# Kernel optimization log

Hardware: AMD Instinct MI355X
Metric: run time of the kernel (lower is better)

The kernel has to match this reference:

```python
import jax, jax.numpy as jnp
import numpy as np

HIDDEN = 4544
N_HEADS = 71
HEAD_DIM = 64
ROPE_BASE = 10000.0


def _rope_cos_sin(pos, dtype):
    # Falcon rotary embedding for a single decode position `pos`.
    inv_freq = 1.0 / (ROPE_BASE ** (jnp.arange(0, HEAD_DIM, 2, dtype=jnp.float32) / HEAD_DIM))
    freqs = pos * inv_freq                      # [HEAD_DIM/2]
    emb = jnp.concatenate([freqs, freqs])       # [HEAD_DIM]
    return jnp.cos(emb).astype(dtype), jnp.sin(emb).astype(dtype)


def _rotate_half(x):
    x1, x2 = jnp.split(x, 2, axis=-1)
    return jnp.concatenate([-x2, x1], axis=-1)


def setup_inputs() -> dict:
    key = jax.random.key(0)
    ks = jax.random.split(key, 6)
    B = 32
    return {
        "hidden_states": jax.random.normal(ks[0], (1, 1, B, HIDDEN), jnp.float32) * 0.02,
        "attention_mask": jnp.zeros((B, 1, 1, 2048), jnp.float32),
        "w_qkv": jax.random.normal(ks[1], (HIDDEN, (N_HEADS + 2) * HEAD_DIM), jnp.float32) * 0.02,
        "w_dense": jax.random.normal(ks[2], (HIDDEN, HIDDEN), jnp.float32) * 0.02,
        "k_cache": jax.random.normal(ks[3], (B, 1, 2048, HEAD_DIM), jnp.float32),
        "v_cache": jax.random.normal(ks[4], (B, 1, 2048, HEAD_DIM), jnp.float32),
        "layer_past_len": 2047,
    }


def reference(hidden_states, attention_mask, w_qkv, w_dense, k_cache, v_cache, layer_past_len):
    B = hidden_states.shape[2]
    kv_len = layer_past_len + 1
    scalar = 1.0 / np.sqrt(HEAD_DIM)

    x = hidden_states.reshape(B, HIDDEN)                    # decode: [1,1,B,H] -> [B,H]
    qkv = x @ w_qkv                                          # [B, (nh+2)*hd]
    q = qkv[:, : N_HEADS * HEAD_DIM].reshape(B, N_HEADS, HEAD_DIM)
    k = qkv[:, N_HEADS * HEAD_DIM : (N_HEADS + 1) * HEAD_DIM]  # [B, hd] (single MQA KV head)
    v = qkv[:, (N_HEADS + 1) * HEAD_DIM :]                     # [B, hd]

    cos, sin = _rope_cos_sin(jnp.float32(layer_past_len), qkv.dtype)
    q = q * cos + _rotate_half(q) * sin                      # [B, nh, hd]
    k = k * cos + _rotate_half(k) * sin                      # [B, hd]

    # KV-cache scatter update at position layer_past_len
    k_cache = k_cache.at[:, 0, layer_past_len, :].set(k)
    v_cache = v_cache.at[:, 0, layer_past_len, :].set(v)

    keys = k_cache[:, 0, :kv_len, :]                         # [B, L, hd]
    vals = v_cache[:, 0, :kv_len, :]                         # [B, L, hd]

    scores = jnp.einsum("bnh,blh->bnl", q, keys) * scalar    # [B, nh, L]
    scores = scores + attention_mask[:, 0, :, :kv_len]       # mask [B,1,L] broadcast over heads
    probs = jax.nn.softmax(scores, axis=-1)
    ctx = jnp.einsum("bnl,blh->bnh", probs, vals)            # [B, nh, hd]

    out = ctx.reshape(B, HIDDEN) @ w_dense                   # [B, H]
    return out.reshape(1, 1, B, HIDDEN)
```

## Files before the change

### kernel.cpp

```cpp
#include <hip/hip_runtime.h>
#include <math.h>

#define BB    32
#define HID   4544
#define NQKV  4672
#define NKT   71
#define KVCAP 2048

__global__ __launch_bounds__(256) void gemm32v4(
    const float* __restrict__ x, const float* __restrict__ W,
    float* __restrict__ part, int N, int KSG)
{
  __shared__ float xT[64 * 32];
  int lane = threadIdx.x & 63;
  int w    = threadIdx.x >> 6;
  int r0   = w * 8;
  int c0   = blockIdx.x * 256 + lane * 4;
  bool act = c0 < N;
  int cb   = act ? c0 : 0;
  int slice = blockIdx.y;

  float acc[8][4];
#pragma unroll
  for (int r = 0; r < 8; ++r)
#pragma unroll
    for (int j = 0; j < 4; ++j) acc[r][j] = 0.f;

  for (int t = slice; t < NKT; t += KSG) {
    int k0 = t * 64;
    __syncthreads();
    {
      int r  = threadIdx.x & 31;
      int kg = threadIdx.x >> 5;
      const float* xp = x + (size_t)r * HID + k0 + kg * 8;
      float4 a = *(const float4*)xp;
      float4 b = *(const float4*)(xp + 4);
      int kk = kg * 8;
      xT[(kk + 0) * 32 + r] = a.x;
      xT[(kk + 1) * 32 + r] = a.y;
      xT[(kk + 2) * 32 + r] = a.z;
      xT[(kk + 3) * 32 + r] = a.w;
      xT[(kk + 4) * 32 + r] = b.x;
      xT[(kk + 5) * 32 + r] = b.y;
      xT[(kk + 6) * 32 + r] = b.z;
      xT[(kk + 7) * 32 + r] = b.w;
    }
    __syncthreads();

    const float* wp = W + (size_t)k0 * N + cb;

#define FMA_STEP(KK, WV)                                                  \
    {                                                                     \
      float4 xa = *(const float4*)&xT[(KK) * 32 + r0];                    \
      float4 xb = *(const float4*)&xT[(KK) * 32 + r0 + 4];                \
      acc[0][0] = fmaf(xa.x, WV.x, acc[0][0]);                            \
      acc[0][1] = fmaf(xa.x, WV.y, acc[0][1]);                            \
      acc[0][2] = fmaf(xa.x, WV.z, acc[0][2]);                            \
      acc[0][3] = fmaf(xa.x, WV.w, acc[0][3]);                            \
      acc[1][0] = fmaf(xa.y, WV.x, acc[1][0]);                            \
      acc[1][1] = fmaf(xa.y, WV.y, acc[1][1]);                            \
      acc[1][2] = fmaf(xa.y, WV.z, acc[1][2]);                            \
      acc[1][3] = fmaf(xa.y, WV.w, acc[1][3]);                            \
      acc[2][0] = fmaf(xa.z, WV.x, acc[2][0]);                            \
      acc[2][1] = fmaf(xa.z, WV.y, acc[2][1]);                            \
      acc[2][2] = fmaf(xa.z, WV.z, acc[2][2]);                            \
      acc[2][3] = fmaf(xa.z, WV.w, acc[2][3]);                            \
      acc[3][0] = fmaf(xa.w, WV.x, acc[3][0]);                            \
      acc[3][1] = fmaf(xa.w, WV.y, acc[3][1]);                            \
      acc[3][2] = fmaf(xa.w, WV.z, acc[3][2]);                            \
      acc[3][3] = fmaf(xa.w, WV.w, acc[3][3]);                            \
      acc[4][0] = fmaf(xb.x, WV.x, acc[4][0]);                            \
      acc[4][1] = fmaf(xb.x, WV.y, acc[4][1]);                            \
      acc[4][2] = fmaf(xb.x, WV.z, acc[4][2]);                            \
      acc[4][3] = fmaf(xb.x, WV.w, acc[4][3]);                            \
      acc[5][0] = fmaf(xb.y, WV.x, acc[5][0]);                            \
      acc[5][1] = fmaf(xb.y, WV.y, acc[5][1]);                            \
      acc[5][2] = fmaf(xb.y, WV.z, acc[5][2]);                            \
      acc[5][3] = fmaf(xb.y, WV.w, acc[5][3]);                            \
      acc[6][0] = fmaf(xb.z, WV.x, acc[6][0]);                            \
      acc[6][1] = fmaf(xb.z, WV.y, acc[6][1]);                            \
      acc[6][2] = fmaf(xb.z, WV.z, acc[6][2]);                            \
      acc[6][3] = fmaf(xb.z, WV.w, acc[6][3]);                            \
      acc[7][0] = fmaf(xb.w, WV.x, acc[7][0]);                            \
      acc[7][1] = fmaf(xb.w, WV.y, acc[7][1]);                            \
      acc[7][2] = fmaf(xb.w, WV.z, acc[7][2]);                            \
      acc[7][3] = fmaf(xb.w, WV.w, acc[7][3]);                            \
    }

#define LOADW(P, KB)                                                      \
    {                                                                     \
      P##0 = *(const float4*)(wp + (size_t)((KB) + 0) * N);               \
      P##1 = *(const float4*)(wp + (size_t)((KB) + 1) * N);               \
      P##2 = *(const float4*)(wp + (size_t)((KB) + 2) * N);               \
      P##3 = *(const float4*)(wp + (size_t)((KB) + 3) * N);               \
    }
#define FMA4(P, KB)                                                       \
    { FMA_STEP((KB) + 0, P##0) FMA_STEP((KB) + 1, P##1)                   \
      FMA_STEP((KB) + 2, P##2) FMA_STEP((KB) + 3, P##3) }

    float4 A0, A1, A2, A3, B0, B1, B2, B3;
    float4 C0, C1, C2, C3, D0, D1, D2, D3;
    LOADW(A, 0) LOADW(B, 4) LOADW(C, 8) LOADW(D, 12)
    FMA4(A, 0)   LOADW(A, 16)
    FMA4(B, 4)   LOADW(B, 20)
    FMA4(C, 8)   LOADW(C, 24)
    FMA4(D, 12)  LOADW(D, 28)
    FMA4(A, 16)  LOADW(A, 32)
    FMA4(B, 20)  LOADW(B, 36)
    FMA4(C, 24)  LOADW(C, 40)
    FMA4(D, 28)  LOADW(D, 44)
    FMA4(A, 32)  LOADW(A, 48)
    FMA4(B, 36)  LOADW(B, 52)
    FMA4(C, 40)  LOADW(C, 56)
    FMA4(D, 44)  LOADW(D, 60)
    FMA4(A, 48)
    FMA4(B, 52)
    FMA4(C, 56)
    FMA4(D, 60)
#undef FMA_STEP
#undef LOADW
#undef FMA4
  }

  if (act) {
#pragma unroll
    for (int r = 0; r < 8; ++r) {
      float4 v = make_float4(acc[r][0], acc[r][1], acc[r][2], acc[r][3]);
      *(float4*)&part[((size_t)slice * 32 + r0 + r) * N + c0] = v;
    }
  }
}

__global__ __launch_bounds__(256) void qkv_fix(
    const float* __restrict__ part, float* __restrict__ qkvr,
    const int* __restrict__ plen, int KSG)
{
  int u = blockIdx.x * 256 + threadIdx.x;
  int r = u / 2368, t = u % 2368;
  int past = *plen;
  const size_t SS = (size_t)32 * NQKV;

  if (t < 2304) {
    int head = t >> 5, j = t & 31;
    int c0 = head * 64 + j;
    int c1 = c0 + 32;
    const float* p = part + (size_t)r * NQKV;
    float av[8], bv[8];
#pragma unroll
    for (int i = 0; i < 8; ++i) { av[i] = 0.f; bv[i] = 0.f; }
    int s = 0;
    for (; s + 8 <= KSG; s += 8)
#pragma unroll
      for (int i = 0; i < 8; ++i) {
        const float* q = p + (size_t)(s + i) * SS;
        av[i] += q[c0]; bv[i] += q[c1];
      }
    for (; s < KSG; ++s) { av[0] += p[(size_t)s * SS + c0]; bv[0] += p[(size_t)s * SS + c1]; }
    float a = ((av[0]+av[1])+(av[2]+av[3])) + ((av[4]+av[5])+(av[6]+av[7]));
    float b = ((bv[0]+bv[1])+(bv[2]+bv[3])) + ((bv[4]+bv[5])+(bv[6]+bv[7]));
    float invf = (float)pow(10000.0, -(double)j / 32.0);
    float fr   = (float)past * invf;
    float cs = (float)cos((double)fr);
    float sn = (float)sin((double)fr);
    float o0 = a * cs - b * sn;
    float o1 = b * cs + a * sn;
    if (head < 71) { o0 *= 0.125f; o1 *= 0.125f; }
    qkvr[(size_t)r * NQKV + c0] = o0;
    qkvr[(size_t)r * NQKV + c1] = o1;
  } else {
    int c = 4608 + (t - 2304);
    const float* p = part + (size_t)r * NQKV + c;
    float av[8];
#pragma unroll
    for (int i = 0; i < 8; ++i) av[i] = 0.f;
    int s = 0;
    for (; s + 8 <= KSG; s += 8)
#pragma unroll
      for (int i = 0; i < 8; ++i) av[i] += p[(size_t)(s + i) * SS];
    for (; s < KSG; ++s) av[0] += p[(size_t)s * SS];
    qkvr[(size_t)r * NQKV + c] =
        ((av[0]+av[1])+(av[2]+av[3])) + ((av[4]+av[5])+(av[6]+av[7]));
  }
}

__global__ __launch_bounds__(256) void attn_part_k(
    const float* __restrict__ qkvr, const float* __restrict__ kc,
    const float* __restrict__ vc,   const float* __restrict__ mask,
    float* __restrict__ part,       const int* __restrict__ plen)
{
  int b     = blockIdx.x;
  int chunk = blockIdx.y;
  int w     = threadIdx.x >> 6;
  int lane  = threadIdx.x & 63;
  int h0    = w * 18;
  int past  = *plen;
  int kvlen = past + 1;
  int pos0  = chunk * 128;

  __shared__ float qsh[4608];
  __shared__ float pls[4][2][64];

  for (int i = threadIdx.x; i < 1152; i += 256) {
    float4 v = (i < 1136) ? ((const float4*)(qkvr + (size_t)b * NQKV))[i]
                          : make_float4(0.f, 0.f, 0.f, 0.f);
    ((float4*)qsh)[i] = v;
  }
  __syncthreads();

  float lh[18], oh[18];
#pragma unroll
  for (int i = 0; i < 18; ++i) { lh[i] = 0.f; oh[i] = 0.f; }

  for (int sub = 0; sub < 2; ++sub) {
    int sp0 = pos0 + sub * 64;
    if (sp0 >= kvlen) break;
    int pos = sp0 + lane;
    bool valid = pos < kvlen;
    const float* krow = (pos == past)
        ? (qkvr + (size_t)b * NQKV + 4544)
        : (kc + ((size_t)b * KVCAP + pos) * 64);
    float4 ka[16];
#pragma unroll
    for (int j = 0; j < 16; ++j) ka[j] = *(const float4*)(krow + j * 4);

    float vv[64];
#pragma unroll
    for (int p = 0; p < 64; ++p) {
      int pp = sp0 + p;
      const float* vrow = (pp == past)
          ? (qkvr + (size_t)b * NQKV + 4608)
          : (vc + ((size_t)b * KVCAP + pp) * 64);
      vv[p] = vrow[lane];
    }
    float mk = valid ? mask[(size_t)b * KVCAP + pos] : 0.f;

#pragma unroll
    for (int i = 0; i < 18; ++i) {
      int h = h0 + i;
      float s0 = 0.f, s1 = 0.f, s2 = 0.f, s3 = 0.f;
#pragma unroll
      for (int j = 0; j < 16; ++j) {
        float4 qv = *(const float4*)&qsh[h * 64 + j * 4];
        s0 = fmaf(ka[j].x, qv.x, s0);
        s1 = fmaf(ka[j].y, qv.y, s1);
        s2 = fmaf(ka[j].z, qv.z, s2);
        s3 = fmaf(ka[j].w, qv.w, s3);
      }
      float s = (s0 + s1) + (s2 + s3) + mk;
      if (!valid) s = -__builtin_inff();
      float p = __expf(s);

      pls[w][i & 1][lane] = p;
      float o0 = 0.f, o1 = 0.f, o2 = 0.f, o3 = 0.f;
      float la = 0.f, lb = 0.f;
#pragma unroll
      for (int j = 0; j < 16; ++j) {
        float4 pr = *(const float4*)&pls[w][i & 1][j * 4];
        o0 = fmaf(pr.x, vv[j * 4 + 0], o0);
        o1 = fmaf(pr.y, vv[j * 4 + 1], o1);
        o2 = fmaf(pr.z, vv[j * 4 + 2], o2);
        o3 = fmaf(pr.w, vv[j * 4 + 3], o3);
        la += pr.x + pr.y;
        lb += pr.z + pr.w;
      }
      oh[i] += (o0 + o1) + (o2 + o3);
      lh[i] += la + lb;
    }
  }

#pragma unroll
  for (int i = 0; i < 18; ++i) {
    int h = h0 + i;
    if (h >= 71) break;
    size_t base = (((size_t)b * 71 + h) * 16 + chunk) * 65;
    if (lane == 0) part[base] = lh[i];
    part[base + 1 + lane] = oh[i];
  }
}

__global__ __launch_bounds__(256) void attn_comb(
    const float* __restrict__ part, float* __restrict__ ctx)
{
  int u = blockIdx.x * 4 + (threadIdx.x >> 6);
  int lane = threadIdx.x & 63;
  if (u >= BB * 71) return;
  float L0 = 0.f, L1 = 0.f, O0 = 0.f, O1 = 0.f;
#pragma unroll
  for (int c = 0; c < 16; c += 2) {
    size_t b0 = ((size_t)u * 16 + c) * 65;
    size_t b1 = ((size_t)u * 16 + c + 1) * 65;
    L0 += part[b0]; O0 += part[b0 + 1 + lane];
    L1 += part[b1]; O1 += part[b1 + 1 + lane];
  }
  int bb = u / 71, h = u % 71;
  ctx[(size_t)bb * HID + h * 64 + lane] = (O0 + O1) / (L0 + L1);
}

__global__ __launch_bounds__(256) void sum_reduce(
    const float* __restrict__ part, float* __restrict__ out, int KSG)
{
  int u4 = blockIdx.x * 256 + threadIdx.x;
  const size_t SS4 = (size_t)32 * HID / 4;
  const float4* p = (const float4*)part + u4;
  float4 a[8];
#pragma unroll
  for (int i = 0; i < 8; ++i) a[i] = make_float4(0.f, 0.f, 0.f, 0.f);
  int s = 0;
  for (; s + 8 <= KSG; s += 8)
#pragma unroll
    for (int i = 0; i < 8; ++i) {
      float4 v = p[(size_t)(s + i) * SS4];
      a[i].x += v.x; a[i].y += v.y; a[i].z += v.z; a[i].w += v.w;
    }
  for (; s < KSG; ++s) {
    float4 v = p[(size_t)s * SS4];
    a[0].x += v.x; a[0].y += v.y; a[0].z += v.z; a[0].w += v.w;
  }
#pragma unroll
  for (int i = 1; i < 8; ++i) {
    a[0].x += a[i].x; a[0].y += a[i].y; a[0].z += a[i].z; a[0].w += a[i].w;
  }
  ((float4*)out)[u4] = a[0];
}

extern "C" void kernel_launch(void* const* d_in, const int* in_sizes, int n_in,
                              void* d_out, int out_size, void* d_ws, size_t ws_size,
                              hipStream_t stream)
{
  const float* x    = (const float*)d_in[0];
  const float* mask = (const float*)d_in[1];
  const float* wqkv = (const float*)d_in[2];
  const float* wd   = (const float*)d_in[3];
  const float* kc   = (const float*)d_in[4];
  const float* vc   = (const float*)d_in[5];
  const int*   pl   = (const int*)d_in[6];
  float* out = (float*)d_out;
  float* ws  = (float*)d_ws;

  size_t wf = ws_size / 4;
  long avail = (long)wf - 294912;
  long slots = avail / 149504;
  int KSG = (int)(slots < 1 ? 1 : (slots > NKT ? NKT : slots));

  size_t partReg = (size_t)KSG * 149504;
  if (partReg < 4795392) partReg = 4795392;
  float* part = ws;
  float* qkvr = ws + partReg;
  float* ctx  = qkvr + 149504;

  gemm32v4   <<<dim3(19, KSG), 256, 0, stream>>>(x, wqkv, part, NQKV, KSG);
  qkv_fix    <<<296,           256, 0, stream>>>(part, qkvr, pl, KSG);
  attn_part_k<<<dim3(32, 16),  256, 0, stream>>>(qkvr, kc, vc, mask, part, pl);
  attn_comb  <<<568,           256, 0, stream>>>(part, ctx);
  gemm32v4   <<<dim3(18, KSG), 256, 0, stream>>>(ctx, wd, part, HID, KSG);
  sum_reduce <<<142,           256, 0, stream>>>(part, out, KSG);
}
```

Baseline: 381.4 us.

## Split attention into 64-position chunks and stage K tile in swizzled shared memory

```diff
diff --git a/kernel.cpp b/kernel.cpp
--- a/kernel.cpp
+++ b/kernel.cpp
@@ -195,9 +195,10 @@
   int h0    = w * 18;
   int past  = *plen;
   int kvlen = past + 1;
-  int pos0  = chunk * 128;
+  int pos0  = chunk * 64;
 
   __shared__ float qsh[4608];
+  __shared__ float ksh[64 * 64];
   __shared__ float pls[4][2][64];
 
   for (int i = threadIdx.x; i < 1152; i += 256) {
@@ -205,76 +206,86 @@
                           : make_float4(0.f, 0.f, 0.f, 0.f);
     ((float4*)qsh)[i] = v;
   }
+  {
+    int pos = threadIdx.x >> 2;
+    int gp  = pos0 + pos;
+    const float* krow = (gp == past)
+        ? (qkvr + (size_t)b * NQKV + 4544)
+        : (kc + ((size_t)b * KVCAP + gp) * 64);
+    int c = threadIdx.x & 3;
+#pragma unroll
+    for (int i = 0; i < 4; ++i) {
+      int lg = c * 4 + i;
+      float4 v = *(const float4*)(krow + lg * 4);
+      int pg = lg ^ (pos & 15);
+      *(float4*)&ksh[pos * 64 + pg * 4] = v;
+    }
+  }
   __syncthreads();
 
-  float lh[18], oh[18];
-#pragma unroll
-  for (int i = 0; i < 18; ++i) { lh[i] = 0.f; oh[i] = 0.f; }
-
-  for (int sub = 0; sub < 2; ++sub) {
-    int sp0 = pos0 + sub * 64;
-    if (sp0 >= kvlen) break;
-    int pos = sp0 + lane;
-    bool valid = pos < kvlen;
-    const float* krow = (pos == past)
-        ? (qkvr + (size_t)b * NQKV + 4544)
-        : (kc + ((size_t)b * KVCAP + pos) * 64);
-    float4 ka[16];
-#pragma unroll
-    for (int j = 0; j < 16; ++j) ka[j] = *(const float4*)(krow + j * 4);
-
-    float vv[64];
-#pragma unroll
-    for (int p = 0; p < 64; ++p) {
-      int pp = sp0 + p;
-      const float* vrow = (pp == past)
-          ? (qkvr + (size_t)b * NQKV + 4608)
-          : (vc + ((size_t)b * KVCAP + pp) * 64);
-      vv[p] = vrow[lane];
-    }
-    float mk = valid ? mask[(size_t)b * KVCAP + pos] : 0.f;
-
-#pragma unroll
+  if (pos0 >= kvlen) {
     for (int i = 0; i < 18; ++i) {
       int h = h0 + i;
-      float s0 = 0.f, s1 = 0.f, s2 = 0.f, s3 = 0.f;
-#pragma unroll
-      for (int j = 0; j < 16; ++j) {
-        float4 qv = *(const float4*)&qsh[h * 64 + j * 4];
-        s0 = fmaf(ka[j].x, qv.x, s0);
-        s1 = fmaf(ka[j].y, qv.y, s1);
-        s2 = fmaf(ka[j].z, qv.z, s2);
-        s3 = fmaf(ka[j].w, qv.w, s3);
-      }
-      float s = (s0 + s1) + (s2 + s3) + mk;
-      if (!valid) s = -__builtin_inff();
-      float p = __expf(s);
-
-      pls[w][i & 1][lane] = p;
-      float o0 = 0.f, o1 = 0.f, o2 = 0.f, o3 = 0.f;
-      float la = 0.f, lb = 0.f;
-#pragma unroll
-      for (int j = 0; j < 16; ++j) {
-        float4 pr = *(const float4*)&pls[w][i & 1][j * 4];
-        o0 = fmaf(pr.x, vv[j * 4 + 0], o0);
-        o1 = fmaf(pr.y, vv[j * 4 + 1], o1);
-        o2 = fmaf(pr.z, vv[j * 4 + 2], o2);
-        o3 = fmaf(pr.w, vv[j * 4 + 3], o3);
-        la += pr.x + pr.y;
-        lb += pr.z + pr.w;
-      }
-      oh[i] += (o0 + o1) + (o2 + o3);
-      lh[i] += la + lb;
-    }
-  }
-
-#pragma unroll
+      if (h >= 71) break;
+      size_t base = (((size_t)b * 71 + h) * 32 + chunk) * 65;
+      if (lane == 0) part[base] = 0.f;
+      part[base + 1 + lane] = 0.f;
+    }
+    return;
+  }
+
+  int pos = pos0 + lane;
+  bool valid = pos < kvlen;
+  float4 ka[16];
+#pragma unroll
+  for (int j = 0; j < 16; ++j)
+    ka[j] = *(const float4*)&ksh[lane * 64 + ((j ^ (lane & 15)) * 4)];
+
+  float vv[64];
+#pragma unroll
+  for (int p = 0; p < 64; ++p) {
+    int pp = pos0 + p;
+    const float* vrow = (pp == past)
+        ? (qkvr + (size_t)b * NQKV + 4608)
+        : (vc + ((size_t)b * KVCAP + pp) * 64);
+    vv[p] = vrow[lane];
+  }
+  float mk = valid ? mask[(size_t)b * KVCAP + pos] : 0.f;
+
+#pragma unroll 2
   for (int i = 0; i < 18; ++i) {
     int h = h0 + i;
-    if (h >= 71) break;
-    size_t base = (((size_t)b * 71 + h) * 16 + chunk) * 65;
-    if (lane == 0) part[base] = lh[i];
-    part[base + 1 + lane] = oh[i];
+    float s0 = 0.f, s1 = 0.f, s2 = 0.f, s3 = 0.f;
+#pragma unroll
+    for (int j = 0; j < 16; ++j) {
+      float4 qv = *(const float4*)&qsh[h * 64 + j * 4];
+      s0 = fmaf(ka[j].x, qv.x, s0);
+      s1 = fmaf(ka[j].y, qv.y, s1);
+      s2 = fmaf(ka[j].z, qv.z, s2);
+      s3 = fmaf(ka[j].w, qv.w, s3);
+    }
+    float s = (s0 + s1) + (s2 + s3) + mk;
+    if (!valid) s = -__builtin_inff();
+    float p = __expf(s);
+
+    pls[w][i & 1][lane] = p;
+    float o0 = 0.f, o1 = 0.f, o2 = 0.f, o3 = 0.f;
+    float la = 0.f, lb = 0.f;
+#pragma unroll
+    for (int j = 0; j < 16; ++j) {
+      float4 pr = *(const float4*)&pls[w][i & 1][j * 4];
+      o0 = fmaf(pr.x, vv[j * 4 + 0], o0);
+      o1 = fmaf(pr.y, vv[j * 4 + 1], o1);
+      o2 = fmaf(pr.z, vv[j * 4 + 2], o2);
+      o3 = fmaf(pr.w, vv[j * 4 + 3], o3);
+      la += pr.x + pr.y;
+      lb += pr.z + pr.w;
+    }
+    if (h < 71) {
+      size_t base = (((size_t)b * 71 + h) * 32 + chunk) * 65;
+      if (lane == 0) part[base] = la + lb;
+      part[base + 1 + lane] = (o0 + o1) + (o2 + o3);
+    }
   }
 }
 
@@ -286,9 +297,9 @@
   if (u >= BB * 71) return;
   float L0 = 0.f, L1 = 0.f, O0 = 0.f, O1 = 0.f;
 #pragma unroll
-  for (int c = 0; c < 16; c += 2) {
-    size_t b0 = ((size_t)u * 16 + c) * 65;
-    size_t b1 = ((size_t)u * 16 + c + 1) * 65;
+  for (int c = 0; c < 32; c += 2) {
+    size_t b0 = ((size_t)u * 32 + c) * 65;
+    size_t b1 = ((size_t)u * 32 + c + 1) * 65;
     L0 += part[b0]; O0 += part[b0 + 1 + lane];
     L1 += part[b1]; O1 += part[b1 + 1 + lane];
   }
@@ -350,7 +361,7 @@
 
   gemm32v4   <<<dim3(19, KSG), 256, 0, stream>>>(x, wqkv, part, NQKV, KSG);
   qkv_fix    <<<296,           256, 0, stream>>>(part, qkvr, pl, KSG);
-  attn_part_k<<<dim3(32, 16),  256, 0, stream>>>(qkvr, kc, vc, mask, part, pl);
+  attn_part_k<<<dim3(32, 32),  256, 0, stream>>>(qkvr, kc, vc, mask, part, pl);
   attn_comb  <<<568,           256, 0, stream>>>(part, ctx);
   gemm32v4   <<<dim3(18, KSG), 256, 0, stream>>>(ctx, wd, part, HID, KSG);
   sum_reduce <<<142,           256, 0, stream>>>(part, out, KSG);
```

New measurement: 335.0 us. -12.2%, faster.
